# Performance work log

Hardware: AMD Instinct MI355X
Metric: run time of the kernel (lower is better)

## Reference

```python
import jax, jax.numpy as jnp
import numpy as np

N_NODES = 100000
N_EDGES = 1600000
N_FEAT = 165
HIDDEN = 128
N_CLASSES = 2
NEG_SLOPE = 0.2


def setup_inputs() -> dict:
    key = jax.random.key(0)
    ks = jax.random.split(key, 16)
    s = 0.05
    return {
        'x': jax.random.normal(ks[0], (N_NODES, N_FEAT), jnp.float32),
        'edge_src': jax.random.randint(ks[1], (N_EDGES,), 0, N_NODES, jnp.int32),
        'edge_dst': jax.random.randint(ks[2], (N_EDGES,), 0, N_NODES, jnp.int32),
        'W1l': jax.random.normal(ks[3], (N_FEAT, HIDDEN), jnp.float32) * s,
        'b1l': jnp.zeros((HIDDEN,), jnp.float32),
        'W1r': jax.random.normal(ks[4], (N_FEAT, HIDDEN), jnp.float32) * s,
        'b1r': jnp.zeros((HIDDEN,), jnp.float32),
        'att1': jax.random.normal(ks[5], (HIDDEN,), jnp.float32) * s,
        'bias1': jnp.zeros((HIDDEN,), jnp.float32),
        'W2l': jax.random.normal(ks[6], (HIDDEN, N_CLASSES), jnp.float32) * s,
        'b2l': jnp.zeros((N_CLASSES,), jnp.float32),
        'W2r': jax.random.normal(ks[7], (HIDDEN, N_CLASSES), jnp.float32) * s,
        'b2r': jnp.zeros((N_CLASSES,), jnp.float32),
        'att2': jax.random.normal(ks[8], (N_CLASSES,), jnp.float32) * s,
        'bias2': jnp.zeros((N_CLASSES,), jnp.float32),
    }


def gatv2_conv(x, src, dst, Wl, bl, Wr, br, att, bias, n_nodes):
    # PyG GATv2Conv, heads=1: x_l for source/message, x_r for target
    xl = x @ Wl + bl            # [N, D_out]
    xr = x @ Wr + br            # [N, D_out]
    e = jax.nn.leaky_relu(xl[src] + xr[dst], NEG_SLOPE)  # [E, D_out]
    score = e @ att             # [E]
    # segment softmax over destination nodes (stable)
    m = jax.ops.segment_max(score, dst, num_segments=n_nodes)
    a = jnp.exp(score - m[dst])
    denom = jax.ops.segment_sum(a, dst, num_segments=n_nodes)
    alpha = a / denom[dst]      # [E]
    out = jax.ops.segment_sum(alpha[:, None] * xl[src], dst, num_segments=n_nodes)
    return out + bias


def reference(x, edge_src, edge_dst, W1l, b1l, W1r, b1r, att1, bias1,
              W2l, b2l, W2r, b2r, att2, bias2):
    n = x.shape[0]
    # GATv2Conv adds self loops by default; every node has >=1 incoming edge
    loops = jnp.arange(n, dtype=edge_src.dtype)
    src = jnp.concatenate([edge_src, loops])
    dst = jnp.concatenate([edge_dst, loops])
    h = gatv2_conv(x, src, dst, W1l, b1l, W1r, b1r, att1, bias1, n)
    h = jax.nn.relu(h)
    # F.dropout with training=False is identity (eval mode)
    out = gatv2_conv(h, src, dst, W2l, b2l, W2r, b2r, att2, bias2, n)
    return out
```

## Files before the change

### kernel.cpp

```cpp
#include <hip/hip_runtime.h>
#include <hip/hip_bf16.h>

#define N_NODES 100000
#define NPAD 100032
#define N_EDGES 1600000
#define ETOT (N_EDGES + N_NODES)
#define NFEAT 165
#define KP 192
#define HID 128
#define NCLS 2
#define NEG 0.2f

#define NBUCK 391
#define CHUNK 4096
#define NCHUNK 416
#define TOT4 ((NBUCK * NCHUNK) / 4)
#define NSB ((TOT4 + 511) / 512)
#define GS_BLOCKS 2048
#define REPACK_BLKS (NPAD / 64)
#define G1TOT (NPAD / 64)
#define G1A 782
#define G1B (G1TOT - G1A)

typedef short bf16x8 __attribute__((ext_vector_type(8)));
typedef float f32x4 __attribute__((ext_vector_type(4)));

#define OFF_FLAG 0
#define OFF_W 16
#define WO_ATT1 42496
#define WO_BIAS1 42624
#define WO_W2L 42752
#define WO_B2L 43008
#define WO_W2R 43010
#define WO_B2R 43266
#define WO_ATT2 43268
#define WO_BIAS2 43270

#define OFF_XB   43392
#define OFF_XP   OFF_XB
#define OFF_WT   (OFF_XB + NPAD * KP / 2)
#define OFF_BCAT (OFF_WT + 256 * KP / 2)
#define OFF_XLB  (OFF_BCAT + 256)
#define OFF_XRB  (OFF_XLB + NPAD * HID / 2)
#define OFF_PAIRS (OFF_XRB + NPAD * HID / 2)
#define OFF_CSR  (OFF_PAIRS + 2 * ETOT)
#define OFF_ROWPTR (OFF_CSR + ETOT)
#define OFF_S    (OFF_ROWPTR + N_NODES + 8)
#define OFF_XL2  (OFF_S + NBUCK * NCHUNK + 8)
#define OFF_XR2  (OFF_XL2 + N_NODES * NCLS)
#define OFF_H    (OFF_XR2 + N_NODES * NCLS)
#define OFF_DL   (OFF_H + N_NODES * HID)
#define OFF_DR   (OFF_DL + NPAD)
#define OFF_W2A  (OFF_DR + NPAD)
#define OFF_BSUM (OFF_W2A + 512)

__device__ __forceinline__ float bload16(unsigned short u) {
    return __uint_as_float(((unsigned)u) << 16);
}

__device__ __forceinline__ float lrelu(float v) {
    return fmaf(0.4f, fabsf(v), 0.6f * v);
}

__device__ __forceinline__ void unpack8(uint4 q, float* f) {
    f[0] = __uint_as_float(q.x << 16); f[1] = __uint_as_float(q.x & 0xffff0000u);
    f[2] = __uint_as_float(q.y << 16); f[3] = __uint_as_float(q.y & 0xffff0000u);
    f[4] = __uint_as_float(q.z << 16); f[5] = __uint_as_float(q.z & 0xffff0000u);
    f[6] = __uint_as_float(q.w << 16); f[7] = __uint_as_float(q.w & 0xffff0000u);
}

__device__ __forceinline__ unsigned short f2b(float f) {
    __hip_bfloat16 b = __float2bfloat16(f);
    return *(unsigned short*)&b;
}

__device__ __forceinline__ unsigned pack2(float a, float b) {
    return (unsigned)f2b(a) | ((unsigned)f2b(b) << 16);
}

__device__ __forceinline__ unsigned detect_flag(const unsigned short* x16, int lane) {
    unsigned short hh = x16[lane];
    unsigned e = (hh >> 7) & 0xFF;
    bool pl = ((hh & 0x7FFF) == 0) || (e >= 100 && e <= 140);
    unsigned long long m = __ballot(pl);
    return (__popcll(m) >= 52) ? 1u : 0u;
}

#define PREP_WT 49152
#define PREP_BC (PREP_WT + 256)
#define PREP_TOT (PREP_BC + 776)
#define PREP_BLKS ((PREP_TOT + 255) / 256)
__global__ void __launch_bounds__(256) k_prep_hist(
        const int* __restrict__ edst, int* __restrict__ bh,
        const unsigned short* __restrict__ x16,
        const void* W1l, const void* b1l, const void* W1r, const void* b1r,
        const void* att1, const void* bias1, const void* W2l, const void* b2l,
        const void* W2r, const void* b2r, const void* att2, const void* bias2,
        unsigned* __restrict__ flagp, unsigned short* __restrict__ wt,
        float* __restrict__ bcat, float* __restrict__ wb,
        float* __restrict__ w2a, unsigned short* __restrict__ xp) {
    __shared__ int hist[NBUCK];
    if (blockIdx.x < NCHUNK) {
        for (int i = threadIdx.x; i < NBUCK; i += 256) hist[i] = 0;
        __syncthreads();
        int base = blockIdx.x * CHUNK;
        for (int i = threadIdx.x; i < CHUNK; i += 256) {
            int e = base + i;
            if (e >= ETOT) break;
            int d = (e < N_EDGES) ? edst[e] : (e - N_EDGES);
            atomicAdd(&hist[d >> 8], 1);
        }
        __syncthreads();
        for (int b = threadIdx.x; b < NBUCK; b += 256)
            bh[b * NCHUNK + blockIdx.x] = hist[b];
        return;
    }
    int lane = threadIdx.x & 63;
    unsigned isbf = detect_flag(x16, lane);
    const float* xf = (const float*)x16;

    if (blockIdx.x >= NCHUNK + PREP_BLKS) {
        int node0 = (blockIdx.x - NCHUNK - PREP_BLKS) * 64;
        for (int i = threadIdx.x; i < 64 * (KP / 8); i += 256) {
            int r = i / (KP / 8);
            int c0 = (i - r * (KP / 8)) * 8;
            int grow = node0 + r;
            unsigned short hh[8];
#pragma unroll
            for (int j = 0; j < 8; j++) {
                int c = c0 + j;
                unsigned short v = 0;
                if (grow < N_NODES && c < NFEAT) {
                    size_t g = (size_t)grow * NFEAT + c;
                    v = isbf ? x16[g] : f2b(xf[g]);
                }
                hh[j] = v;
            }
            uint4 o;
            o.x = (unsigned)hh[0] | ((unsigned)hh[1] << 16);
            o.y = (unsigned)hh[2] | ((unsigned)hh[3] << 16);
            o.z = (unsigned)hh[4] | ((unsigned)hh[5] << 16);
            o.w = (unsigned)hh[6] | ((unsigned)hh[7] << 16);
            *(uint4*)&xp[(size_t)grow * KP + c0] = o;
        }
        return;
    }

    int i = (blockIdx.x - NCHUNK) * 256 + threadIdx.x;
    if (i == 0) *flagp = isbf;
    if (i >= PREP_TOT) return;
    if (i < PREP_WT) {
        int n = i / KP, k = i - n * KP;
        unsigned short v = 0;
        if (k < NFEAT) {
            const void* src = (n < HID) ? W1l : W1r;
            size_t off = (size_t)k * HID + (n & (HID - 1));
            v = isbf ? ((const unsigned short*)src)[off]
                     : f2b(((const float*)src)[off]);
        }
        wt[i] = v;
    } else if (i < PREP_BC) {
        int n = i - PREP_WT;
        const void* src = (n < HID) ? b1l : b1r;
        int off = n & (HID - 1);
        bcat[n] = isbf ? bload16(((const unsigned short*)src)[off])
                       : ((const float*)src)[off];
    } else {
        int j = i - PREP_BC;
        const void* src; int off; int dst;
        if      (j < 128) { src = att1;  off = j;       dst = WO_ATT1 + j; }
        else if (j < 256) { src = bias1; off = j - 128; dst = WO_BIAS1 + (j - 128); }
        else if (j < 512) { src = W2l;   off = j - 256; dst = WO_W2L + (j - 256); }
        else if (j < 514) { src = b2l;   off = j - 512; dst = WO_B2L + (j - 512); }
        else if (j < 770) { src = W2r;   off = j - 514; dst = WO_W2R + (j - 514); }
        else if (j < 772) { src = b2r;   off = j - 770; dst = WO_B2R + (j - 770); }
        else if (j < 774) { src = att2;  off = j - 772; dst = WO_ATT2 + (j - 772); }
        else              { src = bias2; off = j - 774; dst = WO_BIAS2 + (j - 774); }
        float val = isbf ? bload16(((const unsigned short*)src)[off])
                         : ((const float*)src)[off];
        wb[dst] = val;
        if (j >= 256 && j < 512) w2a[j - 256] = val;
        else if (j >= 514 && j < 770) w2a[256 + (j - 514)] = val;
    }
}

__global__ void __launch_bounds__(512) k_scan1(const int* __restrict__ S,
                                               int* __restrict__ bsum) {
    __shared__ int lds[512];
    int t = threadIdx.x;
    int i = blockIdx.x * 512 + t;
    const uint4* S4 = (const uint4*)S;
    int v = 0;
    if (i < TOT4) {
        uint4 q = S4[i];
        v = (int)(q.x + q.y + q.z + q.w);
    }
    lds[t] = v;
    __syncthreads();
    for (int off = 256; off > 0; off >>= 1) {
        if (t < off) lds[t] += lds[t + off];
        __syncthreads();
    }
    if (t == 0) bsum[blockIdx.x] = lds[0];
}

__global__ void __launch_bounds__(128) k_scan2(int* __restrict__ bsum) {
    __shared__ int lds[128];
    int t = threadIdx.x;
    int v = (t < NSB) ? bsum[t] : 0;
    lds[t] = v;
    __syncthreads();
    for (int off = 1; off < 128; off <<= 1) {
        int x = lds[t];
        if (t >= off) x += lds[t - off];
        __syncthreads();
        lds[t] = x;
        __syncthreads();
    }
    if (t < NSB) bsum[t] = (t == 0) ? 0 : lds[t - 1];
}

__global__ void __launch_bounds__(512) k_scan3(int* __restrict__ S,
                                               const int* __restrict__ bsum,
                                               int* __restrict__ rowptr) {
    __shared__ int lds[512];
    int t = threadIdx.x, b = blockIdx.x;
    int i = b * 512 + t;
    uint4* S4 = (uint4*)S;
    uint4 q = {0, 0, 0, 0};
    if (i < TOT4) q = S4[i];
    int s = (int)(q.x + q.y + q.z + q.w);
    lds[t] = s;
    __syncthreads();
    for (int off = 1; off < 512; off <<= 1) {
        int x = lds[t];
        if (t >= off) x += lds[t - off];
        __syncthreads();
        lds[t] = x;
        __syncthreads();
    }
    int excl = ((t == 0) ? 0 : lds[t - 1]) + bsum[b];
    if (i < TOT4) {
        uint4 o;
        o.x = excl;
        o.y = excl + q.x;
        o.z = excl + q.x + q.y;
        o.w = excl + q.x + q.y + q.z;
        S4[i] = o;
    }
    if (b == 0 && t == 0) rowptr[N_NODES] = ETOT;
}

__device__ __forceinline__ void gemm1_tile(
        int node0, int tid, float (*dpart)[64],
        const unsigned short* __restrict__ xp,
        const unsigned short* __restrict__ wt, const float* __restrict__ bcat,
        const float* __restrict__ attp,
        __hip_bfloat16* __restrict__ xlb, __hip_bfloat16* __restrict__ xrb,
        float* __restrict__ dl, float* __restrict__ dr) {
    int wave = tid >> 6, lane = tid & 63;
    int quad = lane >> 4, li = lane & 15;

    bf16x8 wfrag[4][6];
#pragma unroll
    for (int q = 0; q < 4; q++) {
        int n = wave * 64 + q * 16 + li;
#pragma unroll
        for (int kk = 0; kk < 6; kk++)
            wfrag[q][kk] = *(const bf16x8*)&wt[(size_t)n * KP + kk * 32 + quad * 8];
    }
    float4 bv[4], attq4[4];
    int colbase = (wave & 1) * 64;
#pragma unroll
    for (int q = 0; q < 4; q++) {
        bv[q] = *(const float4*)&bcat[wave * 64 + q * 16 + quad * 4];
        attq4[q] = *(const float4*)&attp[colbase + q * 16 + quad * 4];
    }

    for (int mt = 0; mt < 4; mt++) {
        int node = node0 + mt * 16 + li;
        bf16x8 xfrag[6];
#pragma unroll
        for (int kk = 0; kk < 6; kk++)
            xfrag[kk] = *(const bf16x8*)&xp[(size_t)node * KP + kk * 32 + quad * 8];
        __hip_bfloat16* dst = (wave < 2) ? xlb : xrb;
        float dp = 0.f;
#pragma unroll
        for (int q = 0; q < 4; q++) {
            f32x4 a = {0.f, 0.f, 0.f, 0.f};
#pragma unroll
            for (int kk = 0; kk < 6; kk++)
                a = __builtin_amdgcn_mfma_f32_16x16x32_bf16(wfrag[q][kk], xfrag[kk], a, 0, 0, 0);
            float f0 = a[0] + bv[q].x, f1 = a[1] + bv[q].y;
            float f2 = a[2] + bv[q].z, f3 = a[3] + bv[q].w;
            dp = fmaf(f0, attq4[q].x, dp);
            dp = fmaf(f1, attq4[q].y, dp);
            dp = fmaf(f2, attq4[q].z, dp);
            dp = fmaf(f3, attq4[q].w, dp);
            uint2 val = { pack2(f0, f1), pack2(f2, f3) };
            int col = colbase + q * 16 + quad * 4;
            *(uint2*)&dst[(size_t)node * HID + col] = val;
        }
        dp += __shfl_xor(dp, 16);
        dp += __shfl_xor(dp, 32);
        if (lane < 16) dpart[wave][mt * 16 + li] = dp;
    }
    __syncthreads();
    if (tid < 64)
        dl[node0 + tid] = dpart[0][tid] + dpart[1][tid];
    else if (tid < 128)
        dr[node0 + tid - 64] = dpart[2][tid - 64] + dpart[3][tid - 64];
}

__global__ void __launch_bounds__(256) k_scatter_gemm1(
        const int* __restrict__ esrc, const int* __restrict__ edst,
        const int* __restrict__ S, unsigned* __restrict__ pairs,
        const unsigned short* __restrict__ xp,
        const unsigned short* __restrict__ wt, const float* __restrict__ bcat,
        const float* __restrict__ attp,
        __hip_bfloat16* __restrict__ xlb, __hip_bfloat16* __restrict__ xrb,
        float* __restrict__ dl, float* __restrict__ dr) {
    __shared__ union { int cur[NBUCK]; float dpart[4][64]; } u;
    if (blockIdx.x < NCHUNK) {
        for (int i = threadIdx.x; i < NBUCK; i += 256)
            u.cur[i] = S[i * NCHUNK + blockIdx.x];
        __syncthreads();
        int base = blockIdx.x * CHUNK;
        for (int i = threadIdx.x; i < CHUNK; i += 256) {
            int e = base + i;
            if (e >= ETOT) break;
            int s = (e < N_EDGES) ? esrc[e] : (e - N_EDGES);
            int d = (e < N_EDGES) ? edst[e] : (e - N_EDGES);
            int p = atomicAdd(&u.cur[d >> 8], 1);
            pairs[p] = (unsigned)s | ((unsigned)(d & 255) << 24);
        }
        return;
    }
    int node0 = (blockIdx.x - NCHUNK) * 64;
    gemm1_tile(node0, threadIdx.x, u.dpart, xp, wt, bcat, attp,
               xlb, xrb, dl, dr);
}

__global__ void __launch_bounds__(256) k_bsort_gemm1(
        const int* __restrict__ S, const unsigned* __restrict__ pairs,
        int* __restrict__ rowptr, int* __restrict__ csr,
        const unsigned short* __restrict__ xp,
        const unsigned short* __restrict__ wt, const float* __restrict__ bcat,
        const float* __restrict__ attp,
        __hip_bfloat16* __restrict__ xlb, __hip_bfloat16* __restrict__ xrb,
        float* __restrict__ dl, float* __restrict__ dr) {
    __shared__ union { struct { int hist[256]; int cur[256]; } s;
                       float dpart[4][64]; } u;
    int b = blockIdx.x, t = threadIdx.x;
    if (b < NBUCK) {
        int beg = S[b * NCHUNK];
        int end = (b == NBUCK - 1) ? ETOT : S[(b + 1) * NCHUNK];
        u.s.hist[t] = 0;
        __syncthreads();
        for (int j = beg + t; j < end; j += 256)
            atomicAdd(&u.s.hist[pairs[j] >> 24], 1);
        __syncthreads();
        for (int off = 1; off < 256; off <<= 1) {
            int v = u.s.hist[t];
            if (t >= off) v += u.s.hist[t - off];
            __syncthreads();
            u.s.hist[t] = v;
            __syncthreads();
        }
        int excl = (t == 0) ? 0 : u.s.hist[t - 1];
        int node = b * 256 + t;
        if (node < N_NODES) rowptr[node] = beg + excl;
        u.s.cur[t] = beg + excl;
        __syncthreads();
        for (int j = beg + t; j < end; j += 256) {
            unsigned pr = pairs[j];
            int p = atomicAdd(&u.s.cur[pr >> 24], 1);
            csr[p] = (int)(pr & 0xFFFFFFu);
        }
        return;
    }
    int node0 = (G1A + (b - NBUCK)) * 64;
    gemm1_tile(node0, t, u.dpart, xp, wt, bcat, attp, xlb, xrb, dl, dr);
}

__global__ void __launch_bounds__(256) k_gat1(const int* __restrict__ rowptr,
                                              const int* __restrict__ csr,
                                              const __hip_bfloat16* __restrict__ xlb,
                                              const __hip_bfloat16* __restrict__ xrb,
                                              const float* __restrict__ att,
                                              const float* __restrict__ bias,
                                              const float* __restrict__ dotsl,
                                              const float* __restrict__ dotsr,
                                              unsigned short* __restrict__ h16) {
    int wave = threadIdx.x >> 6, lane = threadIdx.x & 63;
    int sub = lane >> 4, li = lane & 15;
    const uint4* __restrict__ xl4 = (const uint4*)xlb;
    const uint4* __restrict__ xr4 = (const uint4*)xrb;
    uint4* __restrict__ h4 = (uint4*)h16;
    float atv[8];
    {
        float4 t0 = ((const float4*)att)[li * 2];
        float4 t1 = ((const float4*)att)[li * 2 + 1];
        atv[0] = 0.4f * t0.x; atv[1] = 0.4f * t0.y;
        atv[2] = 0.4f * t0.z; atv[3] = 0.4f * t0.w;
        atv[4] = 0.4f * t1.x; atv[5] = 0.4f * t1.y;
        atv[6] = 0.4f * t1.z; atv[7] = 0.4f * t1.w;
    }

    for (int d = blockIdx.x * 4 + wave; d < N_NODES; d += GS_BLOCKS * 4) {
        uint4 qr = xr4[d * 16 + li];
        float xrv[8]; unpack8(qr, xrv);
        float drd = dotsr[d];
        int beg = rowptr[d], end = rowptr[d + 1];
        int iters = (end - beg + 3) >> 2;
        float l = 0.f, o[8];
#pragma unroll
        for (int t = 0; t < 8; t++) o[t] = 0.f;

        int j = beg + sub;
        bool valid = j < end;
        int s = valid ? csr[j] : 0;
        uint4 q = xl4[s * 16 + li];
        float dlc = dotsl[s];

        for (int it = 0; it < iters; it++) {
            float c[8]; unpack8(q, c);
            bool v = valid;
            float dle = dlc;
            j += 4;
            valid = j < end;
            int sn = valid ? csr[j] : 0;
            q = xl4[sn * 16 + li];
            dlc = dotsl[sn];

            float pa = 0.f;
#pragma unroll
            for (int t = 0; t < 8; t++) {
                float vv = c[t] + xrv[t];
                pa = fmaf(atv[t], fabsf(vv), pa);
            }
            pa += __shfl_xor(pa, 1);
            pa += __shfl_xor(pa, 2);
            pa += __shfl_xor(pa, 4);
            pa += __shfl_xor(pa, 8);
            float p = fmaf(0.6f, dle + drd, pa);
            float a = v ? __expf(p) : 0.f;
            l += a;
#pragma unroll
            for (int t = 0; t < 8; t++) o[t] = fmaf(a, c[t], o[t]);
        }
        l += __shfl_xor(l, 16);
        l += __shfl_xor(l, 32);
#pragma unroll
        for (int t = 0; t < 8; t++) {
            o[t] += __shfl_xor(o[t], 16);
            o[t] += __shfl_xor(o[t], 32);
        }
        if (sub == 0) {
            float inv = 1.f / l;
            float4 bv0 = ((const float4*)bias)[li * 2];
            float4 bv1 = ((const float4*)bias)[li * 2 + 1];
            float r0 = fmaxf(fmaf(o[0], inv, bv0.x), 0.f);
            float r1 = fmaxf(fmaf(o[1], inv, bv0.y), 0.f);
            float r2 = fmaxf(fmaf(o[2], inv, bv0.z), 0.f);
            float r3 = fmaxf(fmaf(o[3], inv, bv0.w), 0.f);
            float r4 = fmaxf(fmaf(o[4], inv, bv1.x), 0.f);
            float r5 = fmaxf(fmaf(o[5], inv, bv1.y), 0.f);
            float r6 = fmaxf(fmaf(o[6], inv, bv1.z), 0.f);
            float r7 = fmaxf(fmaf(o[7], inv, bv1.w), 0.f);
            uint4 val = { pack2(r0, r1), pack2(r2, r3),
                          pack2(r4, r5), pack2(r6, r7) };
            h4[d * 16 + li] = val;
        }
    }
}

__global__ void __launch_bounds__(256) k_gemm2(const unsigned short* __restrict__ h16,
                                               const float* __restrict__ wb,
                                               const float* __restrict__ w2a,
                                               float* __restrict__ xl2, float* __restrict__ xr2) {
    int wave = threadIdx.x >> 6, lane = threadIdx.x & 63;
    int node = blockIdx.x * 4 + wave;
    if (node >= N_NODES) return;
    unsigned hw = ((const unsigned*)h16)[node * 64 + lane];
    float h0 = __uint_as_float(hw << 16);
    float h1 = __uint_as_float(hw & 0xffff0000u);
    float4 wl = ((const float4*)w2a)[lane];
    float4 wr = ((const float4*)(w2a + 256))[lane];
    float al0 = h0 * wl.x + h1 * wl.z;
    float al1 = h0 * wl.y + h1 * wl.w;
    float ar0 = h0 * wr.x + h1 * wr.z;
    float ar1 = h0 * wr.y + h1 * wr.w;
#pragma unroll
    for (int off = 32; off > 0; off >>= 1) {
        al0 += __shfl_down(al0, off);
        al1 += __shfl_down(al1, off);
        ar0 += __shfl_down(ar0, off);
        ar1 += __shfl_down(ar1, off);
    }
    if (lane == 0) {
        xl2[node * 2 + 0] = al0 + wb[WO_B2L + 0];
        xl2[node * 2 + 1] = al1 + wb[WO_B2L + 1];
        xr2[node * 2 + 0] = ar0 + wb[WO_B2R + 0];
        xr2[node * 2 + 1] = ar1 + wb[WO_B2R + 1];
    }
}

__global__ void __launch_bounds__(256) k_gat2(const int* __restrict__ rowptr,
                                              const int* __restrict__ csr,
                                              const float* __restrict__ xl2,
                                              const float* __restrict__ xr2,
                                              const float* __restrict__ wb,
                                              const unsigned* __restrict__ flag,
                                              void* __restrict__ dout) {
    int t = blockIdx.x * 256 + threadIdx.x;
    int d = t >> 2, part = t & 3;
    if (d >= N_NODES) return;
    float xr0 = xr2[d * 2 + 0], xr1 = xr2[d * 2 + 1];
    float at0 = wb[WO_ATT2], at1 = wb[WO_ATT2 + 1];
    int beg = rowptr[d], end = rowptr[d + 1];
    float l = 0.f, o0 = 0.f, o1 = 0.f;
    for (int j = beg + part; j < end; j += 4) {
        int s = csr[j];
        float b0 = xl2[s * 2 + 0], b1 = xl2[s * 2 + 1];
        float p = at0 * lrelu(b0 + xr0) + at1 * lrelu(b1 + xr1);
        float a = __expf(p);
        l += a;
        o0 = fmaf(a, b0, o0);
        o1 = fmaf(a, b1, o1);
    }
    l += __shfl_xor(l, 1);  o0 += __shfl_xor(o0, 1);  o1 += __shfl_xor(o1, 1);
    l += __shfl_xor(l, 2);  o0 += __shfl_xor(o0, 2);  o1 += __shfl_xor(o1, 2);
    if (part == 0) {
        float inv = 1.f / l;
        float v0 = fmaf(o0, inv, wb[WO_BIAS2 + 0]);
        float v1 = fmaf(o1, inv, wb[WO_BIAS2 + 1]);
        if (*flag) {
            ((__hip_bfloat16*)dout)[d * 2 + 0] = __float2bfloat16(v0);
            ((__hip_bfloat16*)dout)[d * 2 + 1] = __float2bfloat16(v1);
        } else {
            ((float*)dout)[d * 2 + 0] = v0;
            ((float*)dout)[d * 2 + 1] = v1;
        }
    }
}

extern "C" void kernel_launch(void* const* d_in, const int* in_sizes, int n_in,
                              void* d_out, int out_size, void* d_ws, size_t ws_size,
                              hipStream_t stream) {
    char* w = (char*)d_ws;
    unsigned* flag = (unsigned*)(w + (size_t)OFF_FLAG * 4);
    float* wb = (float*)(w + (size_t)OFF_W * 4);
    unsigned short* xp = (unsigned short*)(w + (size_t)OFF_XP * 4);
    unsigned short* wt = (unsigned short*)(w + (size_t)OFF_WT * 4);
    float* bcat = (float*)(w + (size_t)OFF_BCAT * 4);
    __hip_bfloat16* xlb = (__hip_bfloat16*)(w + (size_t)OFF_XLB * 4);
    __hip_bfloat16* xrb = (__hip_bfloat16*)(w + (size_t)OFF_XRB * 4);
    unsigned* pairs = (unsigned*)(w + (size_t)OFF_PAIRS * 4);
    int* csr = (int*)(w + (size_t)OFF_CSR * 4);
    int* rowptr = (int*)(w + (size_t)OFF_ROWPTR * 4);
    int* S = (int*)(w + (size_t)OFF_S * 4);
    float* xl2 = (float*)(w + (size_t)OFF_XL2 * 4);
    float* xr2 = (float*)(w + (size_t)OFF_XR2 * 4);
    unsigned short* h16 = (unsigned short*)(w + (size_t)OFF_H * 4);
    float* dl = (float*)(w + (size_t)OFF_DL * 4);
    float* dr = (float*)(w + (size_t)OFF_DR * 4);
    float* w2a = (float*)(w + (size_t)OFF_W2A * 4);
    int* bsum = (int*)(w + (size_t)OFF_BSUM * 4);
    const int* esrc = (const int*)d_in[1];
    const int* edst = (const int*)d_in[2];

    k_prep_hist<<<NCHUNK + PREP_BLKS + REPACK_BLKS, 256, 0, stream>>>(
        edst, S, (const unsigned short*)d_in[0],
        d_in[3], d_in[4], d_in[5], d_in[6], d_in[7], d_in[8],
        d_in[9], d_in[10], d_in[11], d_in[12], d_in[13], d_in[14],
        flag, wt, bcat, wb, w2a, xp);

    k_scan1<<<NSB, 512, 0, stream>>>(S, bsum);
    k_scan2<<<1, 128, 0, stream>>>(bsum);
    k_scan3<<<NSB, 512, 0, stream>>>(S, bsum, rowptr);

    k_scatter_gemm1<<<NCHUNK + G1A, 256, 0, stream>>>(
        esrc, edst, S, pairs, xp, wt, bcat,
        wb + WO_ATT1, xlb, xrb, dl, dr);

    k_bsort_gemm1<<<NBUCK + G1B, 256, 0, stream>>>(
        S, pairs, rowptr, csr, xp, wt, bcat,
        wb + WO_ATT1, xlb, xrb, dl, dr);

    k_gat1<<<GS_BLOCKS, 256, 0, stream>>>(rowptr, csr, xlb, xrb,
                                          wb + WO_ATT1, wb + WO_BIAS1,
                                          dl, dr, h16);

    k_gemm2<<<(N_NODES + 3) / 4, 256, 0, stream>>>(h16, wb, w2a, xl2, xr2);

    k_gat2<<<(4 * N_NODES + 255) / 256, 256, 0, stream>>>(rowptr, csr, xl2, xr2,
                                                          wb, flag, d_out);
}
```

Measured before the change: 360.1 us.

## Build CSR row pointers from global per-node degree counts with self-loops first

The histogram pass now also counts per-node in-degree with global atomics. Two new kernels scan those counts to produce rowptr directly and write each node's self-loop as the first entry of its CSR row. Self-loops leave the bucketed pairs path, and the per-bucket local histogram and scan in the bucket-sort kernel go away, since that kernel now seeds its cursors from rowptr. In exchange it adds a memset, two kernel launches and 1.6M scattered global atomics.

```diff
diff --git a/kernel.cpp b/kernel.cpp
--- a/kernel.cpp
+++ b/kernel.cpp
@@ -13,9 +13,10 @@
 
 #define NBUCK 391
 #define CHUNK 4096
-#define NCHUNK 416
+#define NCHUNK 392
 #define TOT4 ((NBUCK * NCHUNK) / 4)
 #define NSB ((TOT4 + 511) / 512)
+#define NGRP 196
 #define GS_BLOCKS 2048
 #define REPACK_BLKS (NPAD / 64)
 #define G1TOT (NPAD / 64)
@@ -53,6 +54,8 @@
 #define OFF_DR   (OFF_DL + NPAD)
 #define OFF_W2A  (OFF_DR + NPAD)
 #define OFF_BSUM (OFF_W2A + 512)
+#define OFF_CNT  (OFF_BSUM + 128)
+#define OFF_BS2  (OFF_CNT + N_NODES)
 
 __device__ __forceinline__ float bload16(unsigned short u) {
     return __uint_as_float(((unsigned)u) << 16);
@@ -92,6 +95,7 @@
 #define PREP_BLKS ((PREP_TOT + 255) / 256)
 __global__ void __launch_bounds__(256) k_prep_hist(
         const int* __restrict__ edst, int* __restrict__ bh,
+        int* __restrict__ cnt,
         const unsigned short* __restrict__ x16,
         const void* W1l, const void* b1l, const void* W1r, const void* b1r,
         const void* att1, const void* bias1, const void* W2l, const void* b2l,
@@ -106,9 +110,10 @@
         int base = blockIdx.x * CHUNK;
         for (int i = threadIdx.x; i < CHUNK; i += 256) {
             int e = base + i;
-            if (e >= ETOT) break;
-            int d = (e < N_EDGES) ? edst[e] : (e - N_EDGES);
+            if (e >= N_EDGES) break;
+            int d = edst[e];
             atomicAdd(&hist[d >> 8], 1);
+            atomicAdd(&cnt[d], 1);
         }
         __syncthreads();
         for (int b = threadIdx.x; b < NBUCK; b += 256)
@@ -221,8 +226,7 @@
 }
 
 __global__ void __launch_bounds__(512) k_scan3(int* __restrict__ S,
-                                               const int* __restrict__ bsum,
-                                               int* __restrict__ rowptr) {
+                                               const int* __restrict__ bsum) {
     __shared__ int lds[512];
     int t = threadIdx.x, b = blockIdx.x;
     int i = b * 512 + t;
@@ -248,6 +252,55 @@
         o.w = excl + q.x + q.y + q.z;
         S4[i] = o;
     }
+}
+
+__global__ void __launch_bounds__(512) k_nscan1(const int* __restrict__ cnt,
+                                                int* __restrict__ bs2) {
+    __shared__ int ws[8];
+    int t = threadIdx.x;
+    int n = blockIdx.x * 512 + t;
+    int v = (n < N_NODES) ? cnt[n] : 0;
+    v += __shfl_down(v, 32);
+    v += __shfl_down(v, 16);
+    v += __shfl_down(v, 8);
+    v += __shfl_down(v, 4);
+    v += __shfl_down(v, 2);
+    v += __shfl_down(v, 1);
+    if ((t & 63) == 0) ws[t >> 6] = v;
+    __syncthreads();
+    if (t == 0) {
+        int s = 0;
+#pragma unroll
+        for (int i = 0; i < 8; i++) s += ws[i];
+        bs2[blockIdx.x] = s;
+    }
+}
+
+__global__ void __launch_bounds__(512) k_nscanw(const int* __restrict__ cnt,
+                                                const int* __restrict__ bs2,
+                                                int* __restrict__ rowptr,
+                                                int* __restrict__ csr) {
+    __shared__ int sb[512];
+    __shared__ int loc[512];
+    int t = threadIdx.x, b = blockIdx.x;
+    int n = b * 512 + t;
+    sb[t] = (t < NGRP) ? bs2[t] : 0;
+    loc[t] = (n < N_NODES) ? cnt[n] : 0;
+    __syncthreads();
+    for (int off = 1; off < 512; off <<= 1) {
+        int v1 = sb[t], v2 = loc[t];
+        if (t >= off) { v1 += sb[t - off]; v2 += loc[t - off]; }
+        __syncthreads();
+        sb[t] = v1; loc[t] = v2;
+        __syncthreads();
+    }
+    int base = (b == 0) ? 0 : sb[b - 1];
+    int excl = (t == 0) ? 0 : loc[t - 1];
+    if (n < N_NODES) {
+        int rp = base + excl + n;
+        rowptr[n] = rp;
+        csr[rp] = n;
+    }
     if (b == 0 && t == 0) rowptr[N_NODES] = ETOT;
 }
 
@@ -328,9 +381,8 @@
         int base = blockIdx.x * CHUNK;
         for (int i = threadIdx.x; i < CHUNK; i += 256) {
             int e = base + i;
-            if (e >= ETOT) break;
-            int s = (e < N_EDGES) ? esrc[e] : (e - N_EDGES);
-            int d = (e < N_EDGES) ? edst[e] : (e - N_EDGES);
+            if (e >= N_EDGES) break;
+            int s = esrc[e], d = edst[e];
             int p = atomicAdd(&u.cur[d >> 8], 1);
             pairs[p] = (unsigned)s | ((unsigned)(d & 255) << 24);
         }
@@ -343,38 +395,23 @@
 
 __global__ void __launch_bounds__(256) k_bsort_gemm1(
         const int* __restrict__ S, const unsigned* __restrict__ pairs,
-        int* __restrict__ rowptr, int* __restrict__ csr,
+        const int* __restrict__ rowptr, int* __restrict__ csr,
         const unsigned short* __restrict__ xp,
         const unsigned short* __restrict__ wt, const float* __restrict__ bcat,
         const float* __restrict__ attp,
         __hip_bfloat16* __restrict__ xlb, __hip_bfloat16* __restrict__ xrb,
         float* __restrict__ dl, float* __restrict__ dr) {
-    __shared__ union { struct { int hist[256]; int cur[256]; } s;
-                       float dpart[4][64]; } u;
+    __shared__ union { int cur[256]; float dpart[4][64]; } u;
     int b = blockIdx.x, t = threadIdx.x;
     if (b < NBUCK) {
+        int node = b * 256 + t;
+        u.cur[t] = (node < N_NODES) ? rowptr[node] + 1 : 0;
+        __syncthreads();
         int beg = S[b * NCHUNK];
-        int end = (b == NBUCK - 1) ? ETOT : S[(b + 1) * NCHUNK];
-        u.s.hist[t] = 0;
-        __syncthreads();
-        for (int j = beg + t; j < end; j += 256)
-            atomicAdd(&u.s.hist[pairs[j] >> 24], 1);
-        __syncthreads();
-        for (int off = 1; off < 256; off <<= 1) {
-            int v = u.s.hist[t];
-            if (t >= off) v += u.s.hist[t - off];
-            __syncthreads();
-            u.s.hist[t] = v;
-            __syncthreads();
-        }
-        int excl = (t == 0) ? 0 : u.s.hist[t - 1];
-        int node = b * 256 + t;
-        if (node < N_NODES) rowptr[node] = beg + excl;
-        u.s.cur[t] = beg + excl;
-        __syncthreads();
+        int end = (b == NBUCK - 1) ? N_EDGES : S[(b + 1) * NCHUNK];
         for (int j = beg + t; j < end; j += 256) {
             unsigned pr = pairs[j];
-            int p = atomicAdd(&u.s.cur[pr >> 24], 1);
+            int p = atomicAdd(&u.cur[pr >> 24], 1);
             csr[p] = (int)(pr & 0xFFFFFFu);
         }
         return;
@@ -567,18 +604,25 @@
     float* dr = (float*)(w + (size_t)OFF_DR * 4);
     float* w2a = (float*)(w + (size_t)OFF_W2A * 4);
     int* bsum = (int*)(w + (size_t)OFF_BSUM * 4);
+    int* cnt = (int*)(w + (size_t)OFF_CNT * 4);
+    int* bs2 = (int*)(w + (size_t)OFF_BS2 * 4);
     const int* esrc = (const int*)d_in[1];
     const int* edst = (const int*)d_in[2];
 
+    hipMemsetAsync(cnt, 0, N_NODES * sizeof(int), stream);
+
     k_prep_hist<<<NCHUNK + PREP_BLKS + REPACK_BLKS, 256, 0, stream>>>(
-        edst, S, (const unsigned short*)d_in[0],
+        edst, S, cnt, (const unsigned short*)d_in[0],
         d_in[3], d_in[4], d_in[5], d_in[6], d_in[7], d_in[8],
         d_in[9], d_in[10], d_in[11], d_in[12], d_in[13], d_in[14],
         flag, wt, bcat, wb, w2a, xp);
 
     k_scan1<<<NSB, 512, 0, stream>>>(S, bsum);
     k_scan2<<<1, 128, 0, stream>>>(bsum);
-    k_scan3<<<NSB, 512, 0, stream>>>(S, bsum, rowptr);
+    k_scan3<<<NSB, 512, 0, stream>>>(S, bsum);
+
+    k_nscan1<<<NGRP, 512, 0, stream>>>(cnt, bs2);
+    k_nscanw<<<NGRP, 512, 0, stream>>>(cnt, bs2, rowptr, csr);
 
     k_scatter_gemm1<<<NCHUNK + G1A, 256, 0, stream>>>(
         esrc, edst, S, pairs, xp, wt, bcat,
```

After: 423.4 us. 17.6% more time.
